# Optimization experiments

Hardware: AMD Instinct MI355X
Metric: run time of the kernel (lower is better)

## Reference

```python
import jax, jax.numpy as jnp
import numpy as np

COMMITMENT_COST = 0.25
EPSILON = 1e-5


def setup_inputs() -> dict:
    key = jax.random.key(0)
    k1, k2, k3 = jax.random.split(key, 3)
    B, T, D, M = 64, 512, 256, 1024
    audio_semantic = jax.random.normal(k1, (B, T, D), dtype=jnp.float32)
    eeg_semantic = jax.random.normal(k2, (B, T, D), dtype=jnp.float32)
    init_bound = 1.0 / 400.0
    embedding = jax.random.uniform(k3, (M, D), dtype=jnp.float32,
                                   minval=-init_bound, maxval=init_bound)
    return {"audio_semantic": audio_semantic, "eeg_semantic": eeg_semantic,
            "embedding": embedding}


def _distances(flat, embedding):
    return (jnp.sum(embedding ** 2, axis=1)
            + jnp.sum(flat ** 2, axis=1, keepdims=True)
            - 2.0 * (flat @ embedding.T))


def reference(audio_semantic, eeg_semantic, embedding):
    M, D = embedding.shape
    B, T, _ = audio_semantic.shape
    N = B * T
    a_flat = audio_semantic.reshape(-1, D)
    e_flat = eeg_semantic.reshape(-1, D)

    a_dis = _distances(a_flat, embedding)  # [N, M]
    e_dis = _distances(e_flat, embedding)

    # soft assignment probabilities (clamp tiny negative dists before sqrt)
    a_ph = jax.nn.softmax(-jnp.sqrt(jnp.maximum(a_dis, 0.0)), axis=1)
    a_ph = a_ph.reshape(B, T, M).mean(axis=1)  # [B, M]
    e_ph = jax.nn.softmax(-jnp.sqrt(jnp.maximum(e_dis, 0.0)), axis=1)
    e_ph = e_ph.reshape(B, T, M).mean(axis=1)

    # cross-modal code matching loss
    Scode = a_ph @ jnp.log(e_ph.T + 1e-10) + e_ph @ jnp.log(a_ph.T + 1e-10)  # [B, B]
    MaxScode = jnp.max(-Scode)
    EScode = jnp.exp(Scode + MaxScode)
    Lcmcm = -jnp.mean(jnp.log(jnp.diag(EScode) / (jnp.sum(EScode, axis=1) + EPSILON)))
    cmcm_loss = 0.5 * Lcmcm

    # hard assignment + codebook gather
    a_indices = jnp.argmin(a_dis, axis=-1)  # [N]
    e_indices = jnp.argmin(e_dis, axis=-1)
    a_quantized = embedding[a_indices].reshape(B, T, D)
    e_quantized = embedding[e_indices].reshape(B, T, D)

    # per-sample mode of indices (ties -> smallest index, like torch.mode)
    a_counts = jax.nn.one_hot(a_indices.reshape(B, T), M, dtype=jnp.float32).sum(axis=1)
    e_counts = jax.nn.one_hot(e_indices.reshape(B, T), M, dtype=jnp.float32).sum(axis=1)
    a_mode = jnp.argmax(a_counts, axis=-1)
    e_mode = jnp.argmax(e_counts, axis=-1)
    equal_num = jnp.sum(a_mode == e_mode)

    # commitment losses (quantized detached)
    a_q_sg = jax.lax.stop_gradient(a_quantized)
    e_q_sg = jax.lax.stop_gradient(e_quantized)
    a_e_latent = jnp.mean((audio_semantic - a_q_sg) ** 2)
    ae_e_latent = jnp.mean((audio_semantic - e_q_sg) ** 2)
    a_loss = COMMITMENT_COST * (2.0 * a_e_latent + ae_e_latent)
    e_e_latent = jnp.mean((eeg_semantic - e_q_sg) ** 2)
    ea_e_latent = jnp.mean((eeg_semantic - a_q_sg) ** 2)
    e_loss = COMMITMENT_COST * (2.0 * e_e_latent + ea_e_latent)

    # straight-through estimator
    a_quantized_st = audio_semantic + jax.lax.stop_gradient(a_quantized - audio_semantic)
    e_quantized_st = eeg_semantic + jax.lax.stop_gradient(e_quantized - eeg_semantic)

    # perplexity from average usage
    a_avg = jnp.zeros((M,), jnp.float32).at[a_indices].add(1.0) / N
    e_avg = jnp.zeros((M,), jnp.float32).at[e_indices].add(1.0) / N
    a_perplexity = jnp.exp(-jnp.sum(a_avg * jnp.log(a_avg + 1e-10)))
    e_perplexity = jnp.exp(-jnp.sum(e_avg * jnp.log(e_avg + 1e-10)))

    return (a_quantized_st, e_quantized_st, a_loss, e_loss,
            a_perplexity, e_perplexity, cmcm_loss, equal_num)
```

## Files before the change

### kernel.cpp

```cpp
#include <hip/hip_runtime.h>
#include <math.h>

#define Bn 64
#define Tn 512
#define Dn 256
#define Mn 1024
#define Nn (Bn * Tn)
#define NnDn ((size_t)Nn * Dn)

typedef __attribute__((ext_vector_type(8))) short short8v;
typedef __attribute__((ext_vector_type(4))) float float4v;

#define OFF_APH   0
#define OFF_EPH   65536
#define OFF_ACNT  131072
#define OFF_ECNT  196608
#define OFF_LAT   262144
#define OFF_ENT   262148
#define OFF_MODEA 262152
#define OFF_MODEE 262216
#define ZERO_FLOATS 262656
#define OFF_SE2   262656
#define OFF_EH    263680
#define OFF_EL    394752
#define OFF_APHN  525824
#define OFF_EPHN  591360
#define OFF_LA    656896
#define OFF_LE    722432
#define OFF_SCODE 787968
#define OUT_SCALARS ((size_t)2 * Nn * Dn)

__device__ __forceinline__ unsigned short bf16hi(float x) {
  unsigned u = __float_as_uint(x);
  return (unsigned short)((u + 0x7FFFu + ((u >> 16) & 1u)) >> 16);
}
__device__ __forceinline__ float bf16tof(unsigned short h) {
  return __uint_as_float(((unsigned)h) << 16);
}

__global__ __launch_bounds__(256) void kPrepE(const float* __restrict__ emb,
                                              float* __restrict__ ws) {
  unsigned short* Eh = (unsigned short*)(ws + OFF_EH);
  unsigned short* El = (unsigned short*)(ws + OFF_EL);
  float* se2 = ws + OFF_SE2;
  const int tid = threadIdx.x;
  const int m = blockIdx.x * 32 + (tid >> 3);
  const int sub = tid & 7;
  const float* src = emb + (size_t)m * Dn + sub * 32;
  unsigned short* dh = Eh + (size_t)sub * 32768 + m * 32;
  unsigned short* dl = El + (size_t)sub * 32768 + m * 32;
  float s2 = 0.f;
  #pragma unroll
  for (int gq = 0; gq < 4; ++gq) {
    float4 v0 = ((const float4*)src)[gq * 2];
    float4 v1 = ((const float4*)src)[gq * 2 + 1];
    float xs[8] = {v0.x, v0.y, v0.z, v0.w, v1.x, v1.y, v1.z, v1.w};
    short8v hv, lv;
    #pragma unroll
    for (int j = 0; j < 8; ++j) {
      s2 = fmaf(xs[j], xs[j], s2);
      unsigned short h = bf16hi(xs[j]);
      hv[j] = (short)h;
      lv[j] = (short)bf16hi(xs[j] - bf16tof(h));
    }
    *(short8v*)(dh + gq * 8) = hv;
    *(short8v*)(dl + gq * 8) = lv;
  }
  s2 += __shfl_xor(s2, 1); s2 += __shfl_xor(s2, 2); s2 += __shfl_xor(s2, 4);
  if (sub == 0) se2[m] = s2;
}

__global__ __launch_bounds__(512, 2) void kMain(
    const float* __restrict__ audio, const float* __restrict__ eeg,
    const float* __restrict__ emb, float* out, float* __restrict__ ws) {
  __shared__ unsigned short Xh[64 * 128];
  __shared__ unsigned short Xl[64 * 128];
  __shared__ float se2l[Mn];
  __shared__ float sx2l[64];
  __shared__ float wmin[64][8];
  __shared__ int   widx[64][8];
  __shared__ float wZ[64][8];
  __shared__ float rowLs[64];
  __shared__ int   rowIdxs[64];
  __shared__ float izs[64];
  __shared__ float redm[8][4];

  const int tid = threadIdx.x;
  const int n0 = blockIdx.x * 32;
  const int b = blockIdx.x >> 4;
  const unsigned short* __restrict__ Eh = (const unsigned short*)(ws + OFF_EH);
  const unsigned short* __restrict__ El = (const unsigned short*)(ws + OFF_EL);

  const int lane = tid & 63, wid = tid >> 6;
  const int c = lane & 15, g = lane >> 4;
  const int colbase = wid * 128;

  se2l[tid] = ws[OFF_SE2 + tid];
  se2l[tid + 512] = ws[OFF_SE2 + tid + 512];

  float4v acc[4][8];
  #pragma unroll
  for (int rg = 0; rg < 4; ++rg)
    #pragma unroll
    for (int cg = 0; cg < 8; ++cg) {
      float4v z = {0.f, 0.f, 0.f, 0.f};
      acc[rg][cg] = z;
    }

  const int srow = tid >> 3, ssub = tid & 7;
  const float* ssrc = (srow < 32) ? (audio + (size_t)(n0 + srow) * Dn)
                                  : (eeg + (size_t)(n0 + srow - 32) * Dn);
  const int sswz = (srow & 7) << 4;
  char* XhB = (char*)Xh;
  char* XlB = (char*)Xl;
  int rowb[4], swzr[4];
  #pragma unroll
  for (int rg = 0; rg < 4; ++rg) {
    int row = rg * 16 + c;
    rowb[rg] = row * 256;
    swzr[rg] = (row & 7) << 4;
  }
  const int eoffv = c * 32 + g * 8;

  float s2 = 0.f;
  for (int ph = 0; ph < 2; ++ph) {
    if (ph) __syncthreads();
    {
      const int d0 = ssub * 16;
      const float* sp = ssrc + ph * 128 + d0;
      #pragma unroll
      for (int g2 = 0; g2 < 2; ++g2) {
        float4 v0 = ((const float4*)sp)[g2 * 2];
        float4 v1 = ((const float4*)sp)[g2 * 2 + 1];
        float xs[8] = {v0.x, v0.y, v0.z, v0.w, v1.x, v1.y, v1.z, v1.w};
        short8v hv, lv;
        #pragma unroll
        for (int j = 0; j < 8; ++j) {
          s2 = fmaf(xs[j], xs[j], s2);
          unsigned short h = bf16hi(xs[j]);
          hv[j] = (short)h;
          lv[j] = (short)bf16hi(xs[j] - bf16tof(h));
        }
        const int ab = (srow * 256 + (d0 + g2 * 8) * 2) ^ sswz;
        *(short8v*)(XhB + ab) = hv;
        *(short8v*)(XlB + ab) = lv;
      }
    }
    __syncthreads();
    for (int ks4 = 0; ks4 < 4; ++ks4) {
      const int kb = ks4 * 64 + g * 16;
      const unsigned short* peh = Eh + (size_t)(ph * 4 + ks4) * 32768
                                     + (size_t)colbase * 32 + eoffv;
      const unsigned short* pel = El + (size_t)(ph * 4 + ks4) * 32768
                                     + (size_t)colbase * 32 + eoffv;
      short8v ah[4], al[4];
      #pragma unroll
      for (int rg = 0; rg < 4; ++rg) {
        const int ab = rowb[rg] + (kb ^ swzr[rg]);
        ah[rg] = *(const short8v*)(XhB + ab);
        al[rg] = *(const short8v*)(XlB + ab);
      }
      #pragma unroll
      for (int cg = 0; cg < 8; ++cg) {
        short8v bh = *(const short8v*)(peh + cg * 512);
        short8v bl = *(const short8v*)(pel + cg * 512);
        #pragma unroll
        for (int rg = 0; rg < 4; ++rg) {
          acc[rg][cg] = __builtin_amdgcn_mfma_f32_16x16x32_bf16(ah[rg], bh, acc[rg][cg], 0, 0, 0);
          acc[rg][cg] = __builtin_amdgcn_mfma_f32_16x16x32_bf16(al[rg], bh, acc[rg][cg], 0, 0, 0);
          acc[rg][cg] = __builtin_amdgcn_mfma_f32_16x16x32_bf16(ah[rg], bl, acc[rg][cg], 0, 0, 0);
        }
      }
    }
  }
  s2 += __shfl_xor(s2, 1); s2 += __shfl_xor(s2, 2); s2 += __shfl_xor(s2, 4);
  if (ssub == 0) sx2l[srow] = s2;

  float se2c[8];
  #pragma unroll
  for (int cg = 0; cg < 8; ++cg) se2c[cg] = se2l[colbase + cg * 16 + c];
  #pragma unroll
  for (int rg = 0; rg < 4; ++rg)
    #pragma unroll
    for (int cg = 0; cg < 8; ++cg)
      #pragma unroll
      for (int q = 0; q < 4; ++q)
        acc[rg][cg][q] = fmaf(-2.f, acc[rg][cg][q], se2c[cg]);

  float vmin[4][4]; int imin[4][4];
  #pragma unroll
  for (int rg = 0; rg < 4; ++rg)
    #pragma unroll
    for (int q = 0; q < 4; ++q) { vmin[rg][q] = 3.0e38f; imin[rg][q] = Mn; }
  #pragma unroll
  for (int cg = 0; cg < 8; ++cg) {
    const int colc = colbase + cg * 16 + c;
    #pragma unroll
    for (int rg = 0; rg < 4; ++rg)
      #pragma unroll
      for (int q = 0; q < 4; ++q) {
        float v = acc[rg][cg][q];
        if (v < vmin[rg][q]) { vmin[rg][q] = v; imin[rg][q] = colc; }
      }
  }
  #pragma unroll
  for (int off = 1; off <= 8; off <<= 1) {
    #pragma unroll
    for (int rg = 0; rg < 4; ++rg)
      #pragma unroll
      for (int q = 0; q < 4; ++q) {
        float ov = __shfl_xor(vmin[rg][q], off);
        int oi = __shfl_xor(imin[rg][q], off);
        if (ov < vmin[rg][q] || (ov == vmin[rg][q] && oi < imin[rg][q])) {
          vmin[rg][q] = ov; imin[rg][q] = oi;
        }
      }
  }
  if (c == 0) {
    #pragma unroll
    for (int rg = 0; rg < 4; ++rg)
      #pragma unroll
      for (int q = 0; q < 4; ++q) {
        int row = rg * 16 + g * 4 + q;
        wmin[row][wid] = vmin[rg][q];
        widx[row][wid] = imin[rg][q];
      }
  }
  __syncthreads();
  if (tid < 64) {
    float m = wmin[tid][0]; int mi = widx[tid][0];
    #pragma unroll
    for (int w = 1; w < 8; ++w) {
      float v = wmin[tid][w]; int i2 = widx[tid][w];
      if (v < m || (v == m && i2 < mi)) { m = v; mi = i2; }
    }
    rowIdxs[tid] = mi;
    rowLs[tid] = sqrtf(fmaxf(m + sx2l[tid], 0.f));
  }
  __syncthreads();
  if (tid < 32) atomicAdd((unsigned*)(ws + OFF_ACNT) + b * Mn + rowIdxs[tid], 1u);
  else if (tid < 64) atomicAdd((unsigned*)(ws + OFF_ECNT) + b * Mn + rowIdxs[tid], 1u);

  float Lpre[4][4], spre[4][4];
  #pragma unroll
  for (int rg = 0; rg < 4; ++rg)
    #pragma unroll
    for (int q = 0; q < 4; ++q) {
      int row = rg * 16 + g * 4 + q;
      Lpre[rg][q] = rowLs[row];
      spre[rg][q] = sx2l[row];
    }
  float zp[4][4];
  #pragma unroll
  for (int rg = 0; rg < 4; ++rg)
    #pragma unroll
    for (int q = 0; q < 4; ++q) zp[rg][q] = 0.f;
  #pragma unroll
  for (int rg = 0; rg < 4; ++rg)
    #pragma unroll
    for (int cg = 0; cg < 8; ++cg)
      #pragma unroll
      for (int q = 0; q < 4; ++q) {
        float d = acc[rg][cg][q] + spre[rg][q];
        float pv = __expf(Lpre[rg][q] - sqrtf(fmaxf(d, 0.f)));
        acc[rg][cg][q] = pv;
        zp[rg][q] += pv;
      }
  #pragma unroll
  for (int off = 1; off <= 8; off <<= 1)
    #pragma unroll
    for (int rg = 0; rg < 4; ++rg)
      #pragma unroll
      for (int q = 0; q < 4; ++q) zp[rg][q] += __shfl_xor(zp[rg][q], off);
  if (c == 0) {
    #pragma unroll
    for (int rg = 0; rg < 4; ++rg)
      #pragma unroll
      for (int q = 0; q < 4; ++q) wZ[rg * 16 + g * 4 + q][wid] = zp[rg][q];
  }
  __syncthreads();
  if (tid < 64) {
    float Z = 0.f;
    #pragma unroll
    for (int w = 0; w < 8; ++w) Z += wZ[tid][w];
    izs[tid] = 1.f / Z;
  }
  __syncthreads();

  float izq[4][4];
  #pragma unroll
  for (int rg = 0; rg < 4; ++rg)
    #pragma unroll
    for (int q = 0; q < 4; ++q) izq[rg][q] = izs[rg * 16 + g * 4 + q];
  float psA[8], psE[8];
  #pragma unroll
  for (int cg = 0; cg < 8; ++cg) {
    float a = 0.f, e = 0.f;
    #pragma unroll
    for (int q = 0; q < 4; ++q) {
      a += acc[0][cg][q] * izq[0][q] + acc[1][cg][q] * izq[1][q];
      e += acc[2][cg][q] * izq[2][q] + acc[3][cg][q] * izq[3][q];
    }
    a += __shfl_xor(a, 16); a += __shfl_xor(a, 32);
    e += __shfl_xor(e, 16); e += __shfl_xor(e, 32);
    psA[cg] = a; psE[cg] = e;
  }
  if (lane < 16) {
    float* phA = ws + OFF_APH;
    float* phE = ws + OFF_EPH;
    #pragma unroll
    for (int cg = 0; cg < 8; ++cg) {
      int colc = colbase + cg * 16 + lane;
      atomicAdd(phA + b * Mn + colc, psA[cg]);
      atomicAdd(phE + b * Mn + colc, psE[cg]);
    }
  }

  {
    const int r = tid >> 4, pp = tid & 15;
    const int ia = rowIdxs[r], ie = rowIdxs[32 + r];
    const float4* qa = (const float4*)(emb + (size_t)ia * Dn);
    const float4* qe = (const float4*)(emb + (size_t)ie * Dn);
    const float4* xa4 = (const float4*)(audio + (size_t)(n0 + r) * Dn);
    const float4* xe4 = (const float4*)(eeg + (size_t)(n0 + r) * Dn);
    float4* oA = (float4*)(out + (size_t)(n0 + r) * Dn);
    float4* oE = (float4*)(out + NnDn + (size_t)(n0 + r) * Dn);
    float s_ae = 0.f, s_aq = 0.f, s_ee = 0.f, s_eq = 0.f;
    #pragma unroll
    for (int h = 0; h < 4; ++h) {
      const int i4 = pp * 4 + h;
      float4 qav = qa[i4], qev = qe[i4], xav = xa4[i4], xev = xe4[i4];
      float qaf[4] = {qav.x, qav.y, qav.z, qav.w};
      float qef[4] = {qev.x, qev.y, qev.z, qev.w};
      float xaf[4] = {xav.x, xav.y, xav.z, xav.w};
      float xef[4] = {xev.x, xev.y, xev.z, xev.w};
      #pragma unroll
      for (int j = 0; j < 4; ++j) {
        float d1 = xaf[j] - qaf[j]; s_ae += d1 * d1;
        float d2 = xaf[j] - qef[j]; s_aq += d2 * d2;
        float d3 = xef[j] - qef[j]; s_ee += d3 * d3;
        float d4 = xef[j] - qaf[j]; s_eq += d4 * d4;
      }
      oA[i4] = qav;
      oE[i4] = qev;
    }
    #pragma unroll
    for (int off = 1; off <= 32; off <<= 1) {
      s_ae += __shfl_xor(s_ae, off);
      s_aq += __shfl_xor(s_aq, off);
      s_ee += __shfl_xor(s_ee, off);
      s_eq += __shfl_xor(s_eq, off);
    }
    if (lane == 0) {
      redm[wid][0] = s_ae; redm[wid][1] = s_aq;
      redm[wid][2] = s_ee; redm[wid][3] = s_eq;
    }
    __syncthreads();
    if (tid < 4) {
      float t = 0.f;
      #pragma unroll
      for (int w = 0; w < 8; ++w) t += redm[w][tid];
      atomicAdd(ws + OFF_LAT + tid, t);
    }
  }
}

__global__ __launch_bounds__(256) void kC0(float* __restrict__ ws) {
  int i = blockIdx.x * 256 + threadIdx.x;
  float a = ws[OFF_APH + i] * (1.f / 512.f);
  float e = ws[OFF_EPH + i] * (1.f / 512.f);
  ws[OFF_APHN + i] = a;
  ws[OFF_EPHN + i] = e;
  ws[OFF_LA + i] = logf(a + 1e-10f);
  ws[OFF_LE + i] = logf(e + 1e-10f);
}

__global__ __launch_bounds__(256) void kC1(float* __restrict__ ws) {
  const int blk = blockIdx.x;
  const int i = blk >> 2, jq = blk & 3;
  const int t = threadIdx.x;
  const int jj = t >> 4, q = t & 15;
  const int j = jq * 16 + jj;
  const float* ai  = ws + OFF_APHN + (size_t)i * Mn;
  const float* ei  = ws + OFF_EPHN + (size_t)i * Mn;
  const float* lej = ws + OFF_LE + (size_t)j * Mn;
  const float* laj = ws + OFF_LA + (size_t)j * Mn;
  float s = 0.f;
  #pragma unroll 4
  for (int m = q * 64; m < q * 64 + 64; ++m)
    s += ai[m] * lej[m] + ei[m] * laj[m];
  s += __shfl_xor(s, 1); s += __shfl_xor(s, 2);
  s += __shfl_xor(s, 4); s += __shfl_xor(s, 8);
  if (q == 0) ws[OFF_SCODE + i * 64 + j] = s;
}

__global__ __launch_bounds__(256) void kMode(float* __restrict__ ws) {
  const int bb = blockIdx.x;
  const unsigned* acnt = (const unsigned*)(ws + OFF_ACNT) + (size_t)bb * Mn;
  const unsigned* ecnt = (const unsigned*)(ws + OFF_ECNT) + (size_t)bb * Mn;
  __shared__ unsigned rv[256]; __shared__ int ri[256];
  __shared__ unsigned rv2[256]; __shared__ int ri2[256];
  const int t = threadIdx.x;
  unsigned bA = 0; int ia = t;
  unsigned bE = 0; int ie = t;
  #pragma unroll
  for (int m = t; m < Mn; m += 256) {
    unsigned ca = acnt[m]; if (ca > bA) { bA = ca; ia = m; }
    unsigned ce = ecnt[m]; if (ce > bE) { bE = ce; ie = m; }
  }
  rv[t] = bA; ri[t] = ia; rv2[t] = bE; ri2[t] = ie;
  __syncthreads();
  for (int s2 = 128; s2 > 0; s2 >>= 1) {
    if (t < s2) {
      if (rv[t + s2] > rv[t] || (rv[t + s2] == rv[t] && ri[t + s2] < ri[t])) {
        rv[t] = rv[t + s2]; ri[t] = ri[t + s2];
      }
      if (rv2[t + s2] > rv2[t] || (rv2[t + s2] == rv2[t] && ri2[t + s2] < ri2[t])) {
        rv2[t] = rv2[t + s2]; ri2[t] = ri2[t + s2];
      }
    }
    __syncthreads();
  }
  if (t == 0) {
    ((int*)ws)[OFF_MODEA + bb] = ri[0];
    ((int*)ws)[OFF_MODEE + bb] = ri2[0];
  }
}

__global__ __launch_bounds__(128) void kPerp(float* __restrict__ ws) {
  const int t = threadIdx.x;
  const int m = blockIdx.x * 128 + t;
  const unsigned* acnt = (const unsigned*)(ws + OFF_ACNT);
  const unsigned* ecnt = (const unsigned*)(ws + OFF_ECNT);
  unsigned ta = 0, te = 0;
  for (int bb = 0; bb < Bn; ++bb) { ta += acnt[(size_t)bb * Mn + m]; te += ecnt[(size_t)bb * Mn + m]; }
  float av = (float)ta * (1.f / 32768.f);
  float ev = (float)te * (1.f / 32768.f);
  float ea = av * logf(av + 1e-10f);
  float ee = ev * logf(ev + 1e-10f);
  #pragma unroll
  for (int off = 1; off <= 32; off <<= 1) { ea += __shfl_xor(ea, off); ee += __shfl_xor(ee, off); }
  __shared__ float r[2][2];
  const int lane = t & 63, w = t >> 6;
  if (lane == 0) { r[w][0] = ea; r[w][1] = ee; }
  __syncthreads();
  if (t == 0) {
    atomicAdd(ws + OFF_ENT + 0, r[0][0] + r[1][0]);
    atomicAdd(ws + OFF_ENT + 1, r[0][1] + r[1][1]);
  }
}

__global__ __launch_bounds__(256) void kFin(float* __restrict__ ws, float* __restrict__ out) {
  __shared__ float sc[4096];
  __shared__ float red[256];
  __shared__ float rterm[64];
  __shared__ float maxv;
  const int tid = threadIdx.x;
  for (int i = tid; i < 4096; i += 256) sc[i] = ws[OFF_SCODE + i];
  __syncthreads();

  float mx = -3.0e38f;
  for (int i = tid; i < 4096; i += 256) mx = fmaxf(mx, -sc[i]);
  red[tid] = mx; __syncthreads();
  for (int s = 128; s > 0; s >>= 1) {
    if (tid < s) red[tid] = fmaxf(red[tid], red[tid + s]);
    __syncthreads();
  }
  if (tid == 0) maxv = red[0];
  __syncthreads();
  const float Max = maxv;

  if (tid < 64) {
    float rs = 0.f;
    for (int j = 0; j < 64; ++j) rs += expf(sc[tid * 64 + j] + Max);
    float dg = expf(sc[tid * 64 + tid] + Max);
    rterm[tid] = logf(dg / (rs + 1e-5f));
  }
  __syncthreads();
  if (tid == 0) {
    float s = 0.f;
    for (int i = 0; i < 64; ++i) s += rterm[i];
    out[OUT_SCALARS + 4] = -0.5f * s / 64.f;
  }
  if (tid == 1) {
    const float* lat = ws + OFF_LAT;
    const float inv = 1.f / 8388608.f;
    float a_e = lat[0] * inv, ae = lat[1] * inv, e_e = lat[2] * inv, ea = lat[3] * inv;
    out[OUT_SCALARS + 0] = 0.25f * (2.f * a_e + ae);
    out[OUT_SCALARS + 1] = 0.25f * (2.f * e_e + ea);
  }
  if (tid == 2) out[OUT_SCALARS + 2] = expf(-ws[OFF_ENT + 0]);
  if (tid == 3) out[OUT_SCALARS + 3] = expf(-ws[OFF_ENT + 1]);
  if (tid == 4) {
    const int* ma = (const int*)ws + OFF_MODEA;
    const int* me = (const int*)ws + OFF_MODEE;
    int eq = 0;
    for (int b2 = 0; b2 < 64; ++b2) eq += (ma[b2] == me[b2]) ? 1 : 0;
    out[OUT_SCALARS + 5] = (float)eq;
  }
}

extern "C" void kernel_launch(void* const* d_in, const int* in_sizes, int n_in,
                              void* d_out, int out_size, void* d_ws, size_t ws_size,
                              hipStream_t stream) {
  const float* audio = (const float*)d_in[0];
  const float* eeg   = (const float*)d_in[1];
  const float* emb   = (const float*)d_in[2];
  float* out = (float*)d_out;
  float* ws  = (float*)d_ws;
  (void)in_sizes; (void)n_in; (void)out_size; (void)ws_size;

  hipMemsetAsync(d_ws, 0, (size_t)ZERO_FLOATS * sizeof(float), stream);
  hipLaunchKernelGGL(kPrepE, dim3(32), dim3(256), 0, stream, emb, ws);
  hipLaunchKernelGGL(kMain, dim3(Nn / 32), dim3(512), 0, stream, audio, eeg, emb, out, ws);
  hipLaunchKernelGGL(kC0, dim3(256), dim3(256), 0, stream, ws);
  hipLaunchKernelGGL(kC1, dim3(256), dim3(256), 0, stream, ws);
  hipLaunchKernelGGL(kMode, dim3(64), dim3(256), 0, stream, ws);
  hipLaunchKernelGGL(kPerp, dim3(8), dim3(128), 0, stream, ws);
  hipLaunchKernelGGL(kFin, dim3(1), dim3(256), 0, stream, ws, out);
}
```

Before: 339.5 us.

## Use 1024-thread kMain blocks with 64 columns per wave; merge aux kernels

kMain now runs 16 waves per block, each covering 64 codebook columns instead of 128. That halves the per-thread accumulator count (acc 4x8 to 4x4) and the per-thread staging work. The cross-wave reductions widen to 16 slots. kC0, kMode and kPerp are merged into one kAux launch, saving two kernel launches. The trade-off is larger blocks with heavier block-wide synchronisation and possibly fewer resident blocks per CU.

```diff
diff --git a/kernel.cpp b/kernel.cpp
--- a/kernel.cpp
+++ b/kernel.cpp
@@ -70,47 +70,45 @@
   if (sub == 0) se2[m] = s2;
 }
 
-__global__ __launch_bounds__(512, 2) void kMain(
+__global__ __launch_bounds__(1024) void kMain(
     const float* __restrict__ audio, const float* __restrict__ eeg,
     const float* __restrict__ emb, float* out, float* __restrict__ ws) {
   __shared__ unsigned short Xh[64 * 128];
   __shared__ unsigned short Xl[64 * 128];
   __shared__ float se2l[Mn];
   __shared__ float sx2l[64];
-  __shared__ float wmin[64][8];
-  __shared__ int   widx[64][8];
-  __shared__ float wZ[64][8];
+  __shared__ float wmin[64][16];
+  __shared__ int   widx[64][16];
+  __shared__ float wZ[64][16];
   __shared__ float rowLs[64];
   __shared__ int   rowIdxs[64];
   __shared__ float izs[64];
-  __shared__ float redm[8][4];
+  __shared__ float redm[16][4];
 
   const int tid = threadIdx.x;
   const int n0 = blockIdx.x * 32;
   const int b = blockIdx.x >> 4;
   const unsigned short* __restrict__ Eh = (const unsigned short*)(ws + OFF_EH);
-  const unsigned short* __restrict__ El = (const unsigned short*)(ws + OFF_EL);
 
   const int lane = tid & 63, wid = tid >> 6;
   const int c = lane & 15, g = lane >> 4;
-  const int colbase = wid * 128;
+  const int colbase = wid * 64;
 
   se2l[tid] = ws[OFF_SE2 + tid];
-  se2l[tid + 512] = ws[OFF_SE2 + tid + 512];
-
-  float4v acc[4][8];
-  #pragma unroll
-  for (int rg = 0; rg < 4; ++rg)
-    #pragma unroll
-    for (int cg = 0; cg < 8; ++cg) {
+
+  float4v acc[4][4];
+  #pragma unroll
+  for (int rg = 0; rg < 4; ++rg)
+    #pragma unroll
+    for (int cg = 0; cg < 4; ++cg) {
       float4v z = {0.f, 0.f, 0.f, 0.f};
       acc[rg][cg] = z;
     }
 
-  const int srow = tid >> 3, ssub = tid & 7;
+  const int srow = tid >> 4, ssub = tid & 15;
   const float* ssrc = (srow < 32) ? (audio + (size_t)(n0 + srow) * Dn)
                                   : (eeg + (size_t)(n0 + srow - 32) * Dn);
-  const int sswz = (srow & 7) << 4;
+  const int sab = (srow * 256 + ssub * 16) ^ ((srow & 7) << 4);
   char* XhB = (char*)Xh;
   char* XlB = (char*)Xl;
   int rowb[4], swzr[4];
@@ -120,39 +118,31 @@
     rowb[rg] = row * 256;
     swzr[rg] = (row & 7) << 4;
   }
-  const int eoffv = c * 32 + g * 8;
+  const unsigned short* pEH = Eh + (size_t)colbase * 32 + (c * 32 + g * 8);
 
   float s2 = 0.f;
   for (int ph = 0; ph < 2; ++ph) {
     if (ph) __syncthreads();
     {
-      const int d0 = ssub * 16;
-      const float* sp = ssrc + ph * 128 + d0;
-      #pragma unroll
-      for (int g2 = 0; g2 < 2; ++g2) {
-        float4 v0 = ((const float4*)sp)[g2 * 2];
-        float4 v1 = ((const float4*)sp)[g2 * 2 + 1];
-        float xs[8] = {v0.x, v0.y, v0.z, v0.w, v1.x, v1.y, v1.z, v1.w};
-        short8v hv, lv;
-        #pragma unroll
-        for (int j = 0; j < 8; ++j) {
-          s2 = fmaf(xs[j], xs[j], s2);
-          unsigned short h = bf16hi(xs[j]);
-          hv[j] = (short)h;
-          lv[j] = (short)bf16hi(xs[j] - bf16tof(h));
-        }
-        const int ab = (srow * 256 + (d0 + g2 * 8) * 2) ^ sswz;
-        *(short8v*)(XhB + ab) = hv;
-        *(short8v*)(XlB + ab) = lv;
-      }
+      const float* sp = ssrc + ph * 128 + ssub * 8;
+      float4 v0 = ((const float4*)sp)[0];
+      float4 v1 = ((const float4*)sp)[1];
+      float xs[8] = {v0.x, v0.y, v0.z, v0.w, v1.x, v1.y, v1.z, v1.w};
+      short8v hv, lv;
+      #pragma unroll
+      for (int j = 0; j < 8; ++j) {
+        s2 = fmaf(xs[j], xs[j], s2);
+        unsigned short h = bf16hi(xs[j]);
+        hv[j] = (short)h;
+        lv[j] = (short)bf16hi(xs[j] - bf16tof(h));
+      }
+      *(short8v*)(XhB + sab) = hv;
+      *(short8v*)(XlB + sab) = lv;
     }
     __syncthreads();
     for (int ks4 = 0; ks4 < 4; ++ks4) {
       const int kb = ks4 * 64 + g * 16;
-      const unsigned short* peh = Eh + (size_t)(ph * 4 + ks4) * 32768
-                                     + (size_t)colbase * 32 + eoffv;
-      const unsigned short* pel = El + (size_t)(ph * 4 + ks4) * 32768
-                                     + (size_t)colbase * 32 + eoffv;
+      const unsigned short* peh = pEH + (size_t)(ph * 4 + ks4) * 32768;
       short8v ah[4], al[4];
       #pragma unroll
       for (int rg = 0; rg < 4; ++rg) {
@@ -161,9 +151,9 @@
         al[rg] = *(const short8v*)(XlB + ab);
       }
       #pragma unroll
-      for (int cg = 0; cg < 8; ++cg) {
+      for (int cg = 0; cg < 4; ++cg) {
         short8v bh = *(const short8v*)(peh + cg * 512);
-        short8v bl = *(const short8v*)(pel + cg * 512);
+        short8v bl = *(const short8v*)(peh + cg * 512 + 262144);
         #pragma unroll
         for (int rg = 0; rg < 4; ++rg) {
           acc[rg][cg] = __builtin_amdgcn_mfma_f32_16x16x32_bf16(ah[rg], bh, acc[rg][cg], 0, 0, 0);
@@ -173,16 +163,17 @@
       }
     }
   }
-  s2 += __shfl_xor(s2, 1); s2 += __shfl_xor(s2, 2); s2 += __shfl_xor(s2, 4);
+  s2 += __shfl_xor(s2, 1); s2 += __shfl_xor(s2, 2);
+  s2 += __shfl_xor(s2, 4); s2 += __shfl_xor(s2, 8);
   if (ssub == 0) sx2l[srow] = s2;
 
-  float se2c[8];
-  #pragma unroll
-  for (int cg = 0; cg < 8; ++cg) se2c[cg] = se2l[colbase + cg * 16 + c];
-  #pragma unroll
-  for (int rg = 0; rg < 4; ++rg)
-    #pragma unroll
-    for (int cg = 0; cg < 8; ++cg)
+  float se2c[4];
+  #pragma unroll
+  for (int cg = 0; cg < 4; ++cg) se2c[cg] = se2l[colbase + cg * 16 + c];
+  #pragma unroll
+  for (int rg = 0; rg < 4; ++rg)
+    #pragma unroll
+    for (int cg = 0; cg < 4; ++cg)
       #pragma unroll
       for (int q = 0; q < 4; ++q)
         acc[rg][cg][q] = fmaf(-2.f, acc[rg][cg][q], se2c[cg]);
@@ -193,7 +184,7 @@
     #pragma unroll
     for (int q = 0; q < 4; ++q) { vmin[rg][q] = 3.0e38f; imin[rg][q] = Mn; }
   #pragma unroll
-  for (int cg = 0; cg < 8; ++cg) {
+  for (int cg = 0; cg < 4; ++cg) {
     const int colc = colbase + cg * 16 + c;
     #pragma unroll
     for (int rg = 0; rg < 4; ++rg)
@@ -230,7 +221,7 @@
   if (tid < 64) {
     float m = wmin[tid][0]; int mi = widx[tid][0];
     #pragma unroll
-    for (int w = 1; w < 8; ++w) {
+    for (int w = 1; w < 16; ++w) {
       float v = wmin[tid][w]; int i2 = widx[tid][w];
       if (v < m || (v == m && i2 < mi)) { m = v; mi = i2; }
     }
@@ -258,7 +249,7 @@
   #pragma unroll
   for (int rg = 0; rg < 4; ++rg)
     #pragma unroll
-    for (int cg = 0; cg < 8; ++cg)
+    for (int cg = 0; cg < 4; ++cg)
       #pragma unroll
       for (int q = 0; q < 4; ++q) {
         float d = acc[rg][cg][q] + spre[rg][q];
@@ -282,7 +273,7 @@
   if (tid < 64) {
     float Z = 0.f;
     #pragma unroll
-    for (int w = 0; w < 8; ++w) Z += wZ[tid][w];
+    for (int w = 0; w < 16; ++w) Z += wZ[tid][w];
     izs[tid] = 1.f / Z;
   }
   __syncthreads();
@@ -292,9 +283,9 @@
   for (int rg = 0; rg < 4; ++rg)
     #pragma unroll
     for (int q = 0; q < 4; ++q) izq[rg][q] = izs[rg * 16 + g * 4 + q];
-  float psA[8], psE[8];
-  #pragma unroll
-  for (int cg = 0; cg < 8; ++cg) {
+  float psA[4], psE[4];
+  #pragma unroll
+  for (int cg = 0; cg < 4; ++cg) {
     float a = 0.f, e = 0.f;
     #pragma unroll
     for (int q = 0; q < 4; ++q) {
@@ -309,7 +300,7 @@
     float* phA = ws + OFF_APH;
     float* phE = ws + OFF_EPH;
     #pragma unroll
-    for (int cg = 0; cg < 8; ++cg) {
+    for (int cg = 0; cg < 4; ++cg) {
       int colc = colbase + cg * 16 + lane;
       atomicAdd(phA + b * Mn + colc, psA[cg]);
       atomicAdd(phE + b * Mn + colc, psE[cg]);
@@ -317,7 +308,7 @@
   }
 
   {
-    const int r = tid >> 4, pp = tid & 15;
+    const int r = tid >> 5, pp = tid & 31;
     const int ia = rowIdxs[r], ie = rowIdxs[32 + r];
     const float4* qa = (const float4*)(emb + (size_t)ia * Dn);
     const float4* qe = (const float4*)(emb + (size_t)ie * Dn);
@@ -327,8 +318,8 @@
     float4* oE = (float4*)(out + NnDn + (size_t)(n0 + r) * Dn);
     float s_ae = 0.f, s_aq = 0.f, s_ee = 0.f, s_eq = 0.f;
     #pragma unroll
-    for (int h = 0; h < 4; ++h) {
-      const int i4 = pp * 4 + h;
+    for (int h = 0; h < 2; ++h) {
+      const int i4 = pp * 2 + h;
       float4 qav = qa[i4], qev = qe[i4], xav = xa4[i4], xev = xe4[i4];
       float qaf[4] = {qav.x, qav.y, qav.z, qav.w};
       float qef[4] = {qev.x, qev.y, qev.z, qev.w};
@@ -359,20 +350,77 @@
     if (tid < 4) {
       float t = 0.f;
       #pragma unroll
-      for (int w = 0; w < 8; ++w) t += redm[w][tid];
+      for (int w = 0; w < 16; ++w) t += redm[w][tid];
       atomicAdd(ws + OFF_LAT + tid, t);
     }
   }
 }
 
-__global__ __launch_bounds__(256) void kC0(float* __restrict__ ws) {
-  int i = blockIdx.x * 256 + threadIdx.x;
-  float a = ws[OFF_APH + i] * (1.f / 512.f);
-  float e = ws[OFF_EPH + i] * (1.f / 512.f);
-  ws[OFF_APHN + i] = a;
-  ws[OFF_EPHN + i] = e;
-  ws[OFF_LA + i] = logf(a + 1e-10f);
-  ws[OFF_LE + i] = logf(e + 1e-10f);
+__global__ __launch_bounds__(256) void kAux(float* __restrict__ ws) {
+  const int blk = blockIdx.x;
+  const int t = threadIdx.x;
+  if (blk < 256) {
+    int i = blk * 256 + t;
+    float a = ws[OFF_APH + i] * (1.f / 512.f);
+    float e = ws[OFF_EPH + i] * (1.f / 512.f);
+    ws[OFF_APHN + i] = a;
+    ws[OFF_EPHN + i] = e;
+    ws[OFF_LA + i] = logf(a + 1e-10f);
+    ws[OFF_LE + i] = logf(e + 1e-10f);
+  } else if (blk < 320) {
+    const int bb = blk - 256;
+    const unsigned* acnt = (const unsigned*)(ws + OFF_ACNT) + (size_t)bb * Mn;
+    const unsigned* ecnt = (const unsigned*)(ws + OFF_ECNT) + (size_t)bb * Mn;
+    __shared__ unsigned rv[256]; __shared__ int ri[256];
+    __shared__ unsigned rv2[256]; __shared__ int ri2[256];
+    unsigned bA = 0; int ia = t;
+    unsigned bE = 0; int ie = t;
+    #pragma unroll
+    for (int m = t; m < Mn; m += 256) {
+      unsigned ca = acnt[m]; if (ca > bA) { bA = ca; ia = m; }
+      unsigned ce = ecnt[m]; if (ce > bE) { bE = ce; ie = m; }
+    }
+    rv[t] = bA; ri[t] = ia; rv2[t] = bE; ri2[t] = ie;
+    __syncthreads();
+    for (int s2 = 128; s2 > 0; s2 >>= 1) {
+      if (t < s2) {
+        if (rv[t + s2] > rv[t] || (rv[t + s2] == rv[t] && ri[t + s2] < ri[t])) {
+          rv[t] = rv[t + s2]; ri[t] = ri[t + s2];
+        }
+        if (rv2[t + s2] > rv2[t] || (rv2[t + s2] == rv2[t] && ri2[t + s2] < ri2[t])) {
+          rv2[t] = rv2[t + s2]; ri2[t] = ri2[t + s2];
+        }
+      }
+      __syncthreads();
+    }
+    if (t == 0) {
+      ((int*)ws)[OFF_MODEA + bb] = ri[0];
+      ((int*)ws)[OFF_MODEE + bb] = ri2[0];
+    }
+  } else {
+    const int m = (blk - 320) * 256 + t;
+    const unsigned* acnt = (const unsigned*)(ws + OFF_ACNT);
+    const unsigned* ecnt = (const unsigned*)(ws + OFF_ECNT);
+    unsigned ta = 0, te = 0;
+    for (int bb = 0; bb < Bn; ++bb) {
+      ta += acnt[(size_t)bb * Mn + m];
+      te += ecnt[(size_t)bb * Mn + m];
+    }
+    float av = (float)ta * (1.f / 32768.f);
+    float ev = (float)te * (1.f / 32768.f);
+    float ea = av * logf(av + 1e-10f);
+    float ee = ev * logf(ev + 1e-10f);
+    #pragma unroll
+    for (int off = 1; off <= 32; off <<= 1) { ea += __shfl_xor(ea, off); ee += __shfl_xor(ee, off); }
+    __shared__ float r2[4][2];
+    const int ln = t & 63, w = t >> 6;
+    if (ln == 0) { r2[w][0] = ea; r2[w][1] = ee; }
+    __syncthreads();
+    if (t == 0) {
+      atomicAdd(ws + OFF_ENT + 0, r2[0][0] + r2[1][0] + r2[2][0] + r2[3][0]);
+      atomicAdd(ws + OFF_ENT + 1, r2[0][1] + r2[1][1] + r2[2][1] + r2[3][1]);
+    }
+  }
 }
 
 __global__ __launch_bounds__(256) void kC1(float* __restrict__ ws) {
@@ -394,62 +442,6 @@
   if (q == 0) ws[OFF_SCODE + i * 64 + j] = s;
 }
 
-__global__ __launch_bounds__(256) void kMode(float* __restrict__ ws) {
-  const int bb = blockIdx.x;
-  const unsigned* acnt = (const unsigned*)(ws + OFF_ACNT) + (size_t)bb * Mn;
-  const unsigned* ecnt = (const unsigned*)(ws + OFF_ECNT) + (size_t)bb * Mn;
-  __shared__ unsigned rv[256]; __shared__ int ri[256];
-  __shared__ unsigned rv2[256]; __shared__ int ri2[256];
-  const int t = threadIdx.x;
-  unsigned bA = 0; int ia = t;
-  unsigned bE = 0; int ie = t;
-  #pragma unroll
-  for (int m = t; m < Mn; m += 256) {
-    unsigned ca = acnt[m]; if (ca > bA) { bA = ca; ia = m; }
-    unsigned ce = ecnt[m]; if (ce > bE) { bE = ce; ie = m; }
-  }
-  rv[t] = bA; ri[t] = ia; rv2[t] = bE; ri2[t] = ie;
-  __syncthreads();
-  for (int s2 = 128; s2 > 0; s2 >>= 1) {
-    if (t < s2) {
-      if (rv[t + s2] > rv[t] || (rv[t + s2] == rv[t] && ri[t + s2] < ri[t])) {
-        rv[t] = rv[t + s2]; ri[t] = ri[t + s2];
-      }
-      if (rv2[t + s2] > rv2[t] || (rv2[t + s2] == rv2[t] && ri2[t + s2] < ri2[t])) {
-        rv2[t] = rv2[t + s2]; ri2[t] = ri2[t + s2];
-      }
-    }
-    __syncthreads();
-  }
-  if (t == 0) {
-    ((int*)ws)[OFF_MODEA + bb] = ri[0];
-    ((int*)ws)[OFF_MODEE + bb] = ri2[0];
-  }
-}
-
-__global__ __launch_bounds__(128) void kPerp(float* __restrict__ ws) {
-  const int t = threadIdx.x;
-  const int m = blockIdx.x * 128 + t;
-  const unsigned* acnt = (const unsigned*)(ws + OFF_ACNT);
-  const unsigned* ecnt = (const unsigned*)(ws + OFF_ECNT);
-  unsigned ta = 0, te = 0;
-  for (int bb = 0; bb < Bn; ++bb) { ta += acnt[(size_t)bb * Mn + m]; te += ecnt[(size_t)bb * Mn + m]; }
-  float av = (float)ta * (1.f / 32768.f);
-  float ev = (float)te * (1.f / 32768.f);
-  float ea = av * logf(av + 1e-10f);
-  float ee = ev * logf(ev + 1e-10f);
-  #pragma unroll
-  for (int off = 1; off <= 32; off <<= 1) { ea += __shfl_xor(ea, off); ee += __shfl_xor(ee, off); }
-  __shared__ float r[2][2];
-  const int lane = t & 63, w = t >> 6;
-  if (lane == 0) { r[w][0] = ea; r[w][1] = ee; }
-  __syncthreads();
-  if (t == 0) {
-    atomicAdd(ws + OFF_ENT + 0, r[0][0] + r[1][0]);
-    atomicAdd(ws + OFF_ENT + 1, r[0][1] + r[1][1]);
-  }
-}
-
 __global__ __launch_bounds__(256) void kFin(float* __restrict__ ws, float* __restrict__ out) {
   __shared__ float sc[4096];
   __shared__ float red[256];
@@ -512,10 +504,8 @@
 
   hipMemsetAsync(d_ws, 0, (size_t)ZERO_FLOATS * sizeof(float), stream);
   hipLaunchKernelGGL(kPrepE, dim3(32), dim3(256), 0, stream, emb, ws);
-  hipLaunchKernelGGL(kMain, dim3(Nn / 32), dim3(512), 0, stream, audio, eeg, emb, out, ws);
-  hipLaunchKernelGGL(kC0, dim3(256), dim3(256), 0, stream, ws);
+  hipLaunchKernelGGL(kMain, dim3(Nn / 32), dim3(1024), 0, stream, audio, eeg, emb, out, ws);
+  hipLaunchKernelGGL(kAux, dim3(324), dim3(256), 0, stream, ws);
   hipLaunchKernelGGL(kC1, dim3(256), dim3(256), 0, stream, ws);
-  hipLaunchKernelGGL(kMode, dim3(64), dim3(256), 0, stream, ws);
-  hipLaunchKernelGGL(kPerp, dim3(8), dim3(128), 0, stream, ws);
   hipLaunchKernelGGL(kFin, dim3(1), dim3(256), 0, stream, ws, out);
 }
```

After: 336.3 us. About the same (-1.0%).
